# Optimization experiments

Hardware: AMD Instinct MI355X
Metric: run time of the kernel (lower is better)

The kernel has to match this reference:

```python
import jax, jax.numpy as jnp
import numpy as np

B, T, D, H = 128, 256, 1024, 1024


def setup_inputs() -> dict:
    key = jax.random.key(0)
    ks = jax.random.split(key, 6)
    s = 0.02
    return {
        "x": jax.random.normal(ks[0], (B, T, D), dtype=jnp.float32),
        "mask": jnp.ones((B, T), dtype=jnp.float32),
        "Wi_f": jax.random.normal(ks[1], (3 * H, D), dtype=jnp.float32) * s,
        "Wh_f": jax.random.normal(ks[2], (3 * H, H), dtype=jnp.float32) * s,
        "bi_f": jnp.zeros((3 * H,), dtype=jnp.float32),
        "bh_f": jnp.zeros((3 * H,), dtype=jnp.float32),
        "Wi_r": jax.random.normal(ks[3], (3 * H, D), dtype=jnp.float32) * s,
        "Wh_r": jax.random.normal(ks[4], (3 * H, H), dtype=jnp.float32) * s,
        "bi_r": jnp.zeros((3 * H,), dtype=jnp.float32),
        "bh_r": jnp.zeros((3 * H,), dtype=jnp.float32),
    }


def _gru_scan(x_tbd, m_tb, Wi, Wh, bi, bh):
    # x_tbd: [T,B,D], m_tb: [T,B]; returns all hidden states [T,B,H]
    h0 = jnp.zeros((x_tbd.shape[1], Wh.shape[1]), dtype=x_tbd.dtype)

    def step(h, inp):
        x_t, m_t = inp
        gi = x_t @ Wi.T + bi          # [B,3H]
        gh = h @ Wh.T + bh            # [B,3H]
        i_r, i_z, i_n = jnp.split(gi, 3, axis=-1)
        h_r, h_z, h_n = jnp.split(gh, 3, axis=-1)
        r = jax.nn.sigmoid(i_r + h_r)
        z = jax.nn.sigmoid(i_z + h_z)
        n = jnp.tanh(i_n + r * h_n)
        h_new = (1.0 - z) * n + z * h
        m = m_t[:, None]
        h_out = m * h_new + (1.0 - m) * h  # masked carry-over
        return h_out, h_out

    _, hs = jax.lax.scan(step, h0, (x_tbd, m_tb))
    return hs


def reference(x, mask, Wi_f, Wh_f, bi_f, bh_f, Wi_r, Wh_r, bi_r, bh_r):
    x_t = jnp.transpose(x, (1, 0, 2))   # [T,B,D]
    m_t = jnp.transpose(mask, (1, 0))   # [T,B]
    hs_f = _gru_scan(x_t, m_t, Wi_f, Wh_f, bi_f, bh_f)              # forward in time
    hs_r = _gru_scan(x_t[::-1], m_t[::-1], Wi_r, Wh_r, bi_r, bh_r)  # reverse in time
    hs_r = hs_r[::-1]
    out = jnp.concatenate([hs_f, hs_r], axis=-1)  # [T,B,2H]
    return jnp.transpose(out, (1, 0, 2))          # [B,T,2H]
```

## Files before the change

kernel.cpp:

```cpp
#include <hip/hip_runtime.h>
#include <hip/hip_bf16.h>

typedef __hip_bfloat16 bf16;
typedef __attribute__((ext_vector_type(8))) short bf16x8;
typedef __attribute__((ext_vector_type(4))) float f32x4;

#define GLDS16(g, l)                                                  \
  __builtin_amdgcn_global_load_lds(                                   \
      (const __attribute__((address_space(1))) void*)(g),             \
      (__attribute__((address_space(3))) void*)(l), 16, 0, 0)

__device__ __forceinline__ float bf2f(bf16 v) { return __bfloat162float(v); }
__device__ __forceinline__ short f2bf(float f) {
  bf16 b = __float2bfloat16(f);
  return *reinterpret_cast<short*>(&b);
}

__global__ __launch_bounds__(256) void cvt_bf16(const float* __restrict__ in,
                                                bf16* __restrict__ out, int n) {
  const int i = (blockIdx.x * 256 + threadIdx.x) * 8;
  if (i >= n) return;
  const float4 u = *(const float4*)(in + i);
  const float4 v = *(const float4*)(in + i + 4);
  bf16x8 w;
  w[0] = f2bf(u.x); w[1] = f2bf(u.y); w[2] = f2bf(u.z); w[3] = f2bf(u.w);
  w[4] = f2bf(v.x); w[5] = f2bf(v.y); w[6] = f2bf(v.z); w[7] = f2bf(v.w);
  *(bf16x8*)(out + i) = w;
}

__global__ __launch_bounds__(256) void cvt_whb(const float* __restrict__ Wh_f,
                                               const float* __restrict__ Wh_r,
                                               bf16* __restrict__ Whb) {
  const int t = blockIdx.x * 256 + threadIdx.x;
  const int d = t / 393216;
  int r = t % 393216;
  const int cg = r / 6144;  r %= 6144;
  const int g = r / 2048;   r %= 2048;
  const int kk = r / 64;
  const int lane = r & 63;
  const float* Wh = d ? Wh_r : Wh_f;
  const int row = g * 1024 + cg * 16 + (lane & 15);
  const int col = kk * 32 + (lane >> 4) * 8;
  const float* s = Wh + (size_t)row * 1024 + col;
  const float4 u = *(const float4*)s;
  const float4 v = *(const float4*)(s + 4);
  bf16x8 w;
  w[0] = f2bf(u.x); w[1] = f2bf(u.y); w[2] = f2bf(u.z); w[3] = f2bf(u.w);
  w[4] = f2bf(v.x); w[5] = f2bf(v.y); w[6] = f2bf(v.z); w[7] = f2bf(v.w);
  *(bf16x8*)(Whb + (size_t)t * 8) = w;
}

__global__ __launch_bounds__(256) void gi_gemm(const bf16* __restrict__ X,
                                               const bf16* __restrict__ Wi,
                                               const float* __restrict__ bi,
                                               bf16* __restrict__ Gi) {
  __shared__ bf16 As[128 * 32];
  __shared__ bf16 Bs[128 * 32];
  const int tid = threadIdx.x;
  const int lane = tid & 63;
  const int w = tid >> 6;
  const int wm = w >> 1, wn = w & 1;
  const int m0 = blockIdx.y * 128;
  const int n0 = blockIdx.x * 128;
  const int rA = lane & 15;
  const int kl = (lane >> 4) * 8;

  f32x4 acc[4][4] = {};

  const bf16* Ab = X + (size_t)m0 * 1024;
  const bf16* Bb = Wi + (size_t)n0 * 1024;

  const int arow = tid >> 2;
  const int akk = (tid & 3) * 8;

  for (int kt = 0; kt < 1024; kt += 32) {
#pragma unroll
    for (int i = 0; i < 2; ++i) {
      GLDS16(Ab + (size_t)(i * 64 + arow) * 1024 + kt + akk,
             As + (i * 256 + w * 64) * 8);
      GLDS16(Bb + (size_t)(i * 64 + arow) * 1024 + kt + akk,
             Bs + (i * 256 + w * 64) * 8);
    }
    asm volatile("s_waitcnt vmcnt(0)" ::: "memory");
    __syncthreads();

    bf16x8 a[4], b[4];
#pragma unroll
    for (int f = 0; f < 4; ++f) {
      a[f] = *(const bf16x8*)(As + (wm * 64 + f * 16 + rA) * 32 + kl);
      b[f] = *(const bf16x8*)(Bs + (wn * 64 + f * 16 + rA) * 32 + kl);
    }
#pragma unroll
    for (int mf = 0; mf < 4; ++mf)
#pragma unroll
      for (int nf = 0; nf < 4; ++nf)
        acc[mf][nf] = __builtin_amdgcn_mfma_f32_16x16x32_bf16(
            a[mf], b[nf], acc[mf][nf], 0, 0, 0);
    __syncthreads();
  }

  const int rgrp = (lane >> 4) * 4;
#pragma unroll
  for (int nf = 0; nf < 4; ++nf) {
    const int col = n0 + wn * 64 + nf * 16 + rA;
    const float bv = bi[col];
#pragma unroll
    for (int mf = 0; mf < 4; ++mf) {
#pragma unroll
      for (int j = 0; j < 4; ++j) {
        const int row = m0 + wm * 64 + mf * 16 + rgrp + j;
        Gi[(size_t)row * 3072 + col] = __float2bfloat16(acc[mf][nf][j] + bv);
      }
    }
  }
}

__global__ __launch_bounds__(256, 1) void gru_persist(
    const bf16* __restrict__ Whb, const float* __restrict__ bh_f,
    const float* __restrict__ bh_r, const bf16* __restrict__ Gi,
    const float* __restrict__ mask, bf16* __restrict__ h16,
    unsigned int* __restrict__ flags, float* __restrict__ out) {
  __shared__ bf16 hs[32 * 1024];
  const int tid = threadIdx.x;
  const int lane = tid & 63;
  const int w = tid >> 6;
  const int mg = w >> 1;
  const int cg = w & 1;
  const int ct = blockIdx.x;
  const int bt = blockIdx.y;
  const int dir = blockIdx.z;
  unsigned int* gflags = flags + (dir * 4 + bt) * 32;

  const float* bh = dir ? bh_r : bh_f;
  const bf16* gi = Gi + (size_t)dir * (32768ull * 3072ull);
  const int bt0 = bt * 32;
  const int c0 = ct * 32;

  const int rA = lane & 15;
  const int klane = lane >> 4;
  const int row = mg * 16 + rA;
  const int colg = c0 + cg * 16 + rA;

  const bf16* bpb = Whb + (size_t)dir * 3145728 +
                    (size_t)((ct * 2 + cg) * 3) * 16384 + lane * 8;
  bf16x8 br[32], bz[32];
#pragma unroll
  for (int kk = 0; kk < 32; ++kk) br[kk] = *(const bf16x8*)(bpb + kk * 512);
#pragma unroll
  for (int kk = 0; kk < 32; ++kk)
    bz[kk] = *(const bf16x8*)(bpb + 16384 + kk * 512);
  const bf16* bpn = bpb + 32768;

  const float bhr = bh[colg];
  const float bhz = bh[1024 + colg];
  const float bhn = bh[2048 + colg];

  float hp[4] = {0.f, 0.f, 0.f, 0.f};
  const int brow0 = bt0 + mg * 16 + klane * 4;

  for (int t = 0; t < 256; ++t) {
    const int p = t & 1;
    const int time = dir ? (255 - t) : t;
    const bf16* hin = h16 + (size_t)(dir * 2 + p) * 131072;
    bf16* hout = h16 + (size_t)(dir * 2 + (p ^ 1)) * 131072;

#pragma unroll
    for (int half = 0; half < 2; ++half) {
      unsigned long long vv[16];
#pragma unroll
      for (int q = 0; q < 16; ++q) {
        const int idx = (half * 16 + q) * 256 + tid;
        const int r = idx >> 8;
        const int c8 = idx & 255;
        vv[q] = __hip_atomic_load(
            (const unsigned long long*)(hin + ((size_t)(bt0 + r) << 10) +
                                        c8 * 4),
            __ATOMIC_RELAXED, __HIP_MEMORY_SCOPE_AGENT);
      }
#pragma unroll
      for (int q = 0; q < 16; ++q) {
        const int idx = (half * 16 + q) * 256 + tid;
        const int r = idx >> 8;
        const int c8 = idx & 255;
        const int ch = c8 >> 1;
        const int sw = ((ch ^ (r & 7)) << 4) | ((c8 & 1) << 3);
        *(unsigned long long*)((char*)hs + r * 2048 + sw) = vv[q];
      }
    }

    float gir[4], giz[4], gin[4], mk[4];
#pragma unroll
    for (int j = 0; j < 4; ++j) {
      const int brow = brow0 + j;
      const size_t gbase = ((size_t)brow * 256 + time) * 3072 + colg;
      gir[j] = bf2f(gi[gbase]);
      giz[j] = bf2f(gi[gbase + 1024]);
      gin[j] = bf2f(gi[gbase + 2048]);
      mk[j] = mask[brow * 256 + time];
    }
    __syncthreads();

    f32x4 acc0 = {}, acc1 = {}, acc2 = {};
#pragma unroll
    for (int kk = 0; kk < 32; ++kk) {
      const int cidx = kk * 4 + klane;
      bf16x8 a = *(const bf16x8*)(hs + row * 1024 + ((cidx ^ (row & 7)) << 3));
      bf16x8 bn = *(const bf16x8*)(bpn + kk * 512);
      acc0 = __builtin_amdgcn_mfma_f32_16x16x32_bf16(a, br[kk], acc0, 0, 0, 0);
      acc1 = __builtin_amdgcn_mfma_f32_16x16x32_bf16(a, bz[kk], acc1, 0, 0, 0);
      acc2 = __builtin_amdgcn_mfma_f32_16x16x32_bf16(a, bn, acc2, 0, 0, 0);
    }

#pragma unroll
    for (int j = 0; j < 4; ++j) {
      const int brow = brow0 + j;
      const float gr = acc0[j] + bhr + gir[j];
      const float gz = acc1[j] + bhz + giz[j];
      const float ghn = acc2[j] + bhn;
      const float r = 1.f / (1.f + __expf(-gr));
      const float z = 1.f / (1.f + __expf(-gz));
      const float nin = gin[j] + r * ghn;
      const float n = 1.f - 2.f / (__expf(2.f * nin) + 1.f);
      float hn = (1.f - z) * n + z * hp[j];
      hn = mk[j] * hn + (1.f - mk[j]) * hp[j];
      hp[j] = hn;
      out[((size_t)brow * 256 + time) * 2048 + (size_t)(dir * 1024) + colg] =
          hn;
      const unsigned short hb = (unsigned short)f2bf(hn);
      const unsigned nb = (unsigned)__shfl_xor((int)hb, 1);
      if (!(lane & 1)) {
        const unsigned dword = (unsigned)hb | (nb << 16);
        __hip_atomic_store(
            (unsigned int*)(hout + ((size_t)brow << 10) + colg), dword,
            __ATOMIC_RELAXED, __HIP_MEMORY_SCOPE_AGENT);
      }
    }

    asm volatile("s_waitcnt vmcnt(0)" ::: "memory");
    __syncthreads();
    if (tid == 0)
      __hip_atomic_store(&gflags[ct], (unsigned)(t + 1), __ATOMIC_RELAXED,
                         __HIP_MEMORY_SCOPE_AGENT);
    if (t < 255) {
      if (w == 0) {
        unsigned v;
        do {
          __builtin_amdgcn_s_sleep(1);
          v = __hip_atomic_load(&gflags[lane & 31], __ATOMIC_RELAXED,
                                __HIP_MEMORY_SCOPE_AGENT);
        } while (__any((int)(v < (unsigned)(t + 1))));
      }
      __builtin_amdgcn_sched_barrier(0);
      __syncthreads();
    }
  }
}

extern "C" void kernel_launch(void* const* d_in, const int* in_sizes, int n_in,
                              void* d_out, int out_size, void* d_ws,
                              size_t ws_size, hipStream_t stream) {
  const float* x = (const float*)d_in[0];
  const float* mask = (const float*)d_in[1];
  const float* Wi_f = (const float*)d_in[2];
  const float* Wh_f = (const float*)d_in[3];
  const float* bi_f = (const float*)d_in[4];
  const float* bh_f = (const float*)d_in[5];
  const float* Wi_r = (const float*)d_in[6];
  const float* Wh_r = (const float*)d_in[7];
  const float* bi_r = (const float*)d_in[8];
  const float* bh_r = (const float*)d_in[9];
  float* out = (float*)d_out;

  char* ws = (char*)d_ws;
  const size_t GI_ELEMS = 32768ull * 3072ull;
  bf16* Gi = (bf16*)ws;
  bf16* Whb = (bf16*)(ws + 2 * GI_ELEMS * sizeof(bf16));
  bf16* h16 = Whb + 2 * 3145728;
  unsigned int* flags = (unsigned int*)(h16 + 4 * 131072);

  bf16* Xb = (bf16*)d_out;
  bf16* Wib_f = Xb + 33554432;
  bf16* Wib_r = Wib_f + 3145728;

  hipMemsetAsync(h16, 0, 4 * 131072 * sizeof(bf16) + 256 * sizeof(unsigned),
                 stream);

  cvt_bf16<<<16384, 256, 0, stream>>>(x, Xb, 33554432);
  cvt_bf16<<<1536, 256, 0, stream>>>(Wi_f, Wib_f, 3145728);
  cvt_bf16<<<1536, 256, 0, stream>>>(Wi_r, Wib_r, 3145728);
  cvt_whb<<<3072, 256, 0, stream>>>(Wh_f, Wh_r, Whb);

  gi_gemm<<<dim3(24, 256), 256, 0, stream>>>(Xb, Wib_f, bi_f, Gi);
  gi_gemm<<<dim3(24, 256), 256, 0, stream>>>(Xb, Wib_r, bi_r, Gi + GI_ELEMS);

  gru_persist<<<dim3(32, 4, 2), 256, 0, stream>>>(Whb, bh_f, bh_r, Gi, mask,
                                                  h16, flags, out);
}
```

Measured before the change: 2.427 ms.

## Split recurrent GRU across 512 smaller blocks and prefetch next-step Gi

```diff
diff --git a/kernel.cpp b/kernel.cpp
--- a/kernel.cpp
+++ b/kernel.cpp
@@ -14,6 +14,19 @@
 __device__ __forceinline__ short f2bf(float f) {
   bf16 b = __float2bfloat16(f);
   return *reinterpret_cast<short*>(&b);
+}
+
+__device__ __forceinline__ unsigned long long ald64(const void* p) {
+  return __hip_atomic_load((const unsigned long long*)p, __ATOMIC_RELAXED,
+                           __HIP_MEMORY_SCOPE_AGENT);
+}
+__device__ __forceinline__ void ast32(void* p, unsigned v) {
+  __hip_atomic_store((unsigned*)p, v, __ATOMIC_RELAXED,
+                     __HIP_MEMORY_SCOPE_AGENT);
+}
+__device__ __forceinline__ unsigned ald32(const void* p) {
+  return __hip_atomic_load((const unsigned*)p, __ATOMIC_RELAXED,
+                           __HIP_MEMORY_SCOPE_AGENT);
 }
 
 __global__ __launch_bounds__(256) void cvt_bf16(const float* __restrict__ in,
@@ -115,11 +128,159 @@
   }
 }
 
-__global__ __launch_bounds__(256, 1) void gru_persist(
+__global__ __launch_bounds__(128, 1) void gru_persist_f(
     const bf16* __restrict__ Whb, const float* __restrict__ bh_f,
     const float* __restrict__ bh_r, const bf16* __restrict__ Gi,
     const float* __restrict__ mask, bf16* __restrict__ h16,
-    unsigned int* __restrict__ flags, float* __restrict__ out) {
+    unsigned* __restrict__ flags, float* __restrict__ out) {
+  __shared__ bf16 hs[32 * 1024];
+  const int tid = threadIdx.x;
+  const int lane = tid & 63;
+  const int w = tid >> 6;
+  const int mg = w;
+  const int bid = blockIdx.x;
+  const int chain = bid & 7;
+  const int ct = bid >> 3;
+  const int dir = chain >> 2;
+  const int bt = chain & 3;
+  unsigned* gflags = flags + chain * 128;
+
+  const float* bh = dir ? bh_r : bh_f;
+  const bf16* gi = Gi + (size_t)dir * (32768ull * 3072ull);
+  const int bt0 = bt * 32;
+  const int rA = lane & 15;
+  const int klane = lane >> 4;
+  const int row = mg * 16 + rA;
+  const int colg = ct * 16 + rA;
+
+  bf16* hbuf0 = h16 + (size_t)(dir * 2 + 0) * 131072;
+  bf16* hbuf1 = h16 + (size_t)(dir * 2 + 1) * 131072;
+
+  const bf16* bp = Whb + (size_t)dir * 3145728 + (size_t)(ct * 3) * 16384 +
+                   lane * 8;
+  bf16x8 br[32], bz[32];
+#pragma unroll
+  for (int kk = 0; kk < 32; ++kk) br[kk] = *(const bf16x8*)(bp + kk * 512);
+#pragma unroll
+  for (int kk = 0; kk < 32; ++kk)
+    bz[kk] = *(const bf16x8*)(bp + 16384 + kk * 512);
+  const bf16* bpn = bp + 32768;
+
+  const float bhr = bh[colg];
+  const float bhz = bh[1024 + colg];
+  const float bhn = bh[2048 + colg];
+
+  float hp[4] = {0.f, 0.f, 0.f, 0.f};
+  const int brow0 = bt0 + mg * 16 + klane * 4;
+
+  float gir[4], giz[4], gin[4], mk4[4];
+  {
+    const int time0 = dir ? 255 : 0;
+#pragma unroll
+    for (int j = 0; j < 4; ++j) {
+      const size_t gbase = ((size_t)(brow0 + j) * 256 + time0) * 3072 + colg;
+      gir[j] = bf2f(gi[gbase]);
+      giz[j] = bf2f(gi[gbase + 1024]);
+      gin[j] = bf2f(gi[gbase + 2048]);
+      mk4[j] = mask[(brow0 + j) * 256 + time0];
+    }
+  }
+
+  for (int t = 0; t < 256; ++t) {
+    const int time = dir ? (255 - t) : t;
+    bf16* hin = (t & 1) ? hbuf1 : hbuf0;
+    bf16* hout = (t & 1) ? hbuf0 : hbuf1;
+
+#pragma unroll
+    for (int b4 = 0; b4 < 4; ++b4) {
+      unsigned long long vv[16];
+#pragma unroll
+      for (int q = 0; q < 16; ++q) {
+        const int idx = (b4 * 16 + q) * 128 + tid;
+        const int r = idx >> 8;
+        const int c8 = idx & 255;
+        vv[q] = ald64(hin + ((size_t)(bt0 + r) << 10) + c8 * 4);
+      }
+#pragma unroll
+      for (int q = 0; q < 16; ++q) {
+        const int idx = (b4 * 16 + q) * 128 + tid;
+        const int r = idx >> 8;
+        const int c8 = idx & 255;
+        const int sw = (((c8 >> 1) ^ (r & 7)) << 4) | ((c8 & 1) << 3);
+        *(unsigned long long*)((char*)hs + r * 2048 + sw) = vv[q];
+      }
+    }
+    __syncthreads();
+
+    f32x4 acc0 = {}, acc1 = {}, acc2 = {};
+#pragma unroll
+    for (int kk = 0; kk < 32; ++kk) {
+      const int cidx = kk * 4 + klane;
+      bf16x8 a = *(const bf16x8*)(hs + row * 1024 + ((cidx ^ (row & 7)) << 3));
+      bf16x8 bn = *(const bf16x8*)(bpn + kk * 512);
+      acc0 = __builtin_amdgcn_mfma_f32_16x16x32_bf16(a, br[kk], acc0, 0, 0, 0);
+      acc1 = __builtin_amdgcn_mfma_f32_16x16x32_bf16(a, bz[kk], acc1, 0, 0, 0);
+      acc2 = __builtin_amdgcn_mfma_f32_16x16x32_bf16(a, bn, acc2, 0, 0, 0);
+    }
+
+    float hnv[4];
+#pragma unroll
+    for (int j = 0; j < 4; ++j) {
+      const float gr = acc0[j] + bhr + gir[j];
+      const float gz = acc1[j] + bhz + giz[j];
+      const float ghn = acc2[j] + bhn;
+      const float r = 1.f / (1.f + __expf(-gr));
+      const float z = 1.f / (1.f + __expf(-gz));
+      const float nin = gin[j] + r * ghn;
+      const float n = 1.f - 2.f / (__expf(2.f * nin) + 1.f);
+      float hn = (1.f - z) * n + z * hp[j];
+      hn = mk4[j] * hn + (1.f - mk4[j]) * hp[j];
+      hp[j] = hn;
+      hnv[j] = hn;
+      const unsigned short hb = (unsigned short)f2bf(hn);
+      const unsigned nb = (unsigned)__shfl_xor((int)hb, 1);
+      if (!(lane & 1))
+        ast32(hout + (((size_t)brow0 + j) << 10) + colg,
+              (unsigned)hb | (nb << 16));
+    }
+
+    asm volatile("s_waitcnt vmcnt(0)" ::: "memory");
+    __syncthreads();
+    if (tid == 0) ast32(&gflags[ct], (unsigned)(t + 1));
+
+#pragma unroll
+    for (int j = 0; j < 4; ++j)
+      out[(((size_t)(brow0 + j)) * 256 + time) * 2048 + (size_t)(dir * 1024) +
+          colg] = hnv[j];
+
+    if (t < 255) {
+      const int tn = dir ? (254 - t) : (t + 1);
+#pragma unroll
+      for (int j = 0; j < 4; ++j) {
+        const size_t gbase = ((size_t)(brow0 + j) * 256 + tn) * 3072 + colg;
+        gir[j] = bf2f(gi[gbase]);
+        giz[j] = bf2f(gi[gbase + 1024]);
+        gin[j] = bf2f(gi[gbase + 2048]);
+        mk4[j] = mask[(brow0 + j) * 256 + tn];
+      }
+      if (w == 0) {
+        unsigned v;
+        do {
+          __builtin_amdgcn_s_sleep(1);
+          v = ald32(&gflags[lane]);
+        } while (__any((int)(v < (unsigned)(t + 1))));
+      }
+      __builtin_amdgcn_sched_barrier(0);
+      __syncthreads();
+    }
+  }
+}
+
+__global__ __launch_bounds__(256, 1) void gru_persist_s(
+    const bf16* __restrict__ Whb, const float* __restrict__ bh_f,
+    const float* __restrict__ bh_r, const bf16* __restrict__ Gi,
+    const float* __restrict__ mask, bf16* __restrict__ h16,
+    unsigned* __restrict__ flags, float* __restrict__ out) {
   __shared__ bf16 hs[32 * 1024];
   const int tid = threadIdx.x;
   const int lane = tid & 63;
@@ -129,27 +290,28 @@
   const int ct = blockIdx.x;
   const int bt = blockIdx.y;
   const int dir = blockIdx.z;
-  unsigned int* gflags = flags + (dir * 4 + bt) * 32;
+  unsigned* gflags = flags + (dir * 4 + bt) * 128;
 
   const float* bh = dir ? bh_r : bh_f;
   const bf16* gi = Gi + (size_t)dir * (32768ull * 3072ull);
   const int bt0 = bt * 32;
-  const int c0 = ct * 32;
-
   const int rA = lane & 15;
   const int klane = lane >> 4;
   const int row = mg * 16 + rA;
-  const int colg = c0 + cg * 16 + rA;
-
-  const bf16* bpb = Whb + (size_t)dir * 3145728 +
-                    (size_t)((ct * 2 + cg) * 3) * 16384 + lane * 8;
+  const int colg = ct * 32 + cg * 16 + rA;
+
+  bf16* hbuf0 = h16 + (size_t)(dir * 2 + 0) * 131072;
+  bf16* hbuf1 = h16 + (size_t)(dir * 2 + 1) * 131072;
+
+  const bf16* bp = Whb + (size_t)dir * 3145728 +
+                   (size_t)((ct * 2 + cg) * 3) * 16384 + lane * 8;
   bf16x8 br[32], bz[32];
 #pragma unroll
-  for (int kk = 0; kk < 32; ++kk) br[kk] = *(const bf16x8*)(bpb + kk * 512);
+  for (int kk = 0; kk < 32; ++kk) br[kk] = *(const bf16x8*)(bp + kk * 512);
 #pragma unroll
   for (int kk = 0; kk < 32; ++kk)
-    bz[kk] = *(const bf16x8*)(bpb + 16384 + kk * 512);
-  const bf16* bpn = bpb + 32768;
+    bz[kk] = *(const bf16x8*)(bp + 16384 + kk * 512);
+  const bf16* bpn = bp + 32768;
 
   const float bhr = bh[colg];
   const float bhz = bh[1024 + colg];
@@ -158,11 +320,23 @@
   float hp[4] = {0.f, 0.f, 0.f, 0.f};
   const int brow0 = bt0 + mg * 16 + klane * 4;
 
+  float gir[4], giz[4], gin[4], mk4[4];
+  {
+    const int time0 = dir ? 255 : 0;
+#pragma unroll
+    for (int j = 0; j < 4; ++j) {
+      const size_t gbase = ((size_t)(brow0 + j) * 256 + time0) * 3072 + colg;
+      gir[j] = bf2f(gi[gbase]);
+      giz[j] = bf2f(gi[gbase + 1024]);
+      gin[j] = bf2f(gi[gbase + 2048]);
+      mk4[j] = mask[(brow0 + j) * 256 + time0];
+    }
+  }
+
   for (int t = 0; t < 256; ++t) {
-    const int p = t & 1;
     const int time = dir ? (255 - t) : t;
-    const bf16* hin = h16 + (size_t)(dir * 2 + p) * 131072;
-    bf16* hout = h16 + (size_t)(dir * 2 + (p ^ 1)) * 131072;
+    bf16* hin = (t & 1) ? hbuf1 : hbuf0;
+    bf16* hout = (t & 1) ? hbuf0 : hbuf1;
 
 #pragma unroll
     for (int half = 0; half < 2; ++half) {
@@ -172,31 +346,16 @@
         const int idx = (half * 16 + q) * 256 + tid;
         const int r = idx >> 8;
         const int c8 = idx & 255;
-        vv[q] = __hip_atomic_load(
-            (const unsigned long long*)(hin + ((size_t)(bt0 + r) << 10) +
-                                        c8 * 4),
-            __ATOMIC_RELAXED, __HIP_MEMORY_SCOPE_AGENT);
+        vv[q] = ald64(hin + ((size_t)(bt0 + r) << 10) + c8 * 4);
       }
 #pragma unroll
       for (int q = 0; q < 16; ++q) {
         const int idx = (half * 16 + q) * 256 + tid;
         const int r = idx >> 8;
         const int c8 = idx & 255;
-        const int ch = c8 >> 1;
-        const int sw = ((ch ^ (r & 7)) << 4) | ((c8 & 1) << 3);
+        const int sw = (((c8 >> 1) ^ (r & 7)) << 4) | ((c8 & 1) << 3);
         *(unsigned long long*)((char*)hs + r * 2048 + sw) = vv[q];
       }
-    }
-
-    float gir[4], giz[4], gin[4], mk[4];
-#pragma unroll
-    for (int j = 0; j < 4; ++j) {
-      const int brow = brow0 + j;
-      const size_t gbase = ((size_t)brow * 256 + time) * 3072 + colg;
-      gir[j] = bf2f(gi[gbase]);
-      giz[j] = bf2f(gi[gbase + 1024]);
-      gin[j] = bf2f(gi[gbase + 2048]);
-      mk[j] = mask[brow * 256 + time];
     }
     __syncthreads();
 
@@ -211,9 +370,9 @@
       acc2 = __builtin_amdgcn_mfma_f32_16x16x32_bf16(a, bn, acc2, 0, 0, 0);
     }
 
+    float hnv[4];
 #pragma unroll
     for (int j = 0; j < 4; ++j) {
-      const int brow = brow0 + j;
       const float gr = acc0[j] + bhr + gir[j];
       const float gz = acc1[j] + bhz + giz[j];
       const float ghn = acc2[j] + bhn;
@@ -222,32 +381,40 @@
       const float nin = gin[j] + r * ghn;
       const float n = 1.f - 2.f / (__expf(2.f * nin) + 1.f);
       float hn = (1.f - z) * n + z * hp[j];
-      hn = mk[j] * hn + (1.f - mk[j]) * hp[j];
+      hn = mk4[j] * hn + (1.f - mk4[j]) * hp[j];
       hp[j] = hn;
-      out[((size_t)brow * 256 + time) * 2048 + (size_t)(dir * 1024) + colg] =
-          hn;
+      hnv[j] = hn;
       const unsigned short hb = (unsigned short)f2bf(hn);
       const unsigned nb = (unsigned)__shfl_xor((int)hb, 1);
-      if (!(lane & 1)) {
-        const unsigned dword = (unsigned)hb | (nb << 16);
-        __hip_atomic_store(
-            (unsigned int*)(hout + ((size_t)brow << 10) + colg), dword,
-            __ATOMIC_RELAXED, __HIP_MEMORY_SCOPE_AGENT);
-      }
+      if (!(lane & 1))
+        ast32(hout + (((size_t)brow0 + j) << 10) + colg,
+              (unsigned)hb | (nb << 16));
     }
 
     asm volatile("s_waitcnt vmcnt(0)" ::: "memory");
     __syncthreads();
-    if (tid == 0)
-      __hip_atomic_store(&gflags[ct], (unsigned)(t + 1), __ATOMIC_RELAXED,
-                         __HIP_MEMORY_SCOPE_AGENT);
+    if (tid == 0) ast32(&gflags[ct], (unsigned)(t + 1));
+
+#pragma unroll
+    for (int j = 0; j < 4; ++j)
+      out[(((size_t)(brow0 + j)) * 256 + time) * 2048 + (size_t)(dir * 1024) +
+          colg] = hnv[j];
+
     if (t < 255) {
+      const int tn = dir ? (254 - t) : (t + 1);
+#pragma unroll
+      for (int j = 0; j < 4; ++j) {
+        const size_t gbase = ((size_t)(brow0 + j) * 256 + tn) * 3072 + colg;
+        gir[j] = bf2f(gi[gbase]);
+        giz[j] = bf2f(gi[gbase + 1024]);
+        gin[j] = bf2f(gi[gbase + 2048]);
+        mk4[j] = mask[(brow0 + j) * 256 + tn];
+      }
       if (w == 0) {
         unsigned v;
         do {
           __builtin_amdgcn_s_sleep(1);
-          v = __hip_atomic_load(&gflags[lane & 31], __ATOMIC_RELAXED,
-                                __HIP_MEMORY_SCOPE_AGENT);
+          v = ald32(&gflags[lane & 31]);
         } while (__any((int)(v < (unsigned)(t + 1))));
       }
       __builtin_amdgcn_sched_barrier(0);
@@ -276,14 +443,13 @@
   bf16* Gi = (bf16*)ws;
   bf16* Whb = (bf16*)(ws + 2 * GI_ELEMS * sizeof(bf16));
   bf16* h16 = Whb + 2 * 3145728;
-  unsigned int* flags = (unsigned int*)(h16 + 4 * 131072);
+  unsigned* flags = (unsigned*)((char*)h16 + 1048576);
 
   bf16* Xb = (bf16*)d_out;
   bf16* Wib_f = Xb + 33554432;
   bf16* Wib_r = Wib_f + 3145728;
 
-  hipMemsetAsync(h16, 0, 4 * 131072 * sizeof(bf16) + 256 * sizeof(unsigned),
-                 stream);
+  hipMemsetAsync(h16, 0, 1048576 + 4096, stream);
 
   cvt_bf16<<<16384, 256, 0, stream>>>(x, Xb, 33554432);
   cvt_bf16<<<1536, 256, 0, stream>>>(Wi_f, Wib_f, 3145728);
@@ -293,6 +459,13 @@
   gi_gemm<<<dim3(24, 256), 256, 0, stream>>>(Xb, Wib_f, bi_f, Gi);
   gi_gemm<<<dim3(24, 256), 256, 0, stream>>>(Xb, Wib_r, bi_r, Gi + GI_ELEMS);
 
-  gru_persist<<<dim3(32, 4, 2), 256, 0, stream>>>(Whb, bh_f, bh_r, Gi, mask,
-                                                  h16, flags, out);
-}
+  int occ = 0;
+  (void)hipOccupancyMaxActiveBlocksPerMultiprocessor(&occ, gru_persist_f, 128,
+                                                     0);
+  if (occ >= 2)
+    gru_persist_f<<<dim3(512), 128, 0, stream>>>(Whb, bh_f, bh_r, Gi, mask,
+                                                 h16, flags, out);
+  else
+    gru_persist_s<<<dim3(32, 4, 2), 256, 0, stream>>>(Whb, bh_f, bh_r, Gi,
+                                                      mask, h16, flags, out);
+}
```

Result: slower. 2.479 ms (+2.1%).
